# Kernel optimization log

Measured on AMD Instinct MI355X. Metric: run time of the kernel, lower is better.

Reference implementation:

```python
import math
import jax, jax.numpy as jnp
import numpy as np

B = 1024
D = 384
Q = 65536
TOPK = 128
HARD_W = 2.0
TEMP_START = 0.2
TEMP_END = 0.05
WARMUP = 10


def _temperature(epoch):
    # curriculum cosine decay (epoch is a Python int)
    if epoch >= WARMUP:
        return TEMP_END
    progress = epoch / max(1, WARMUP)
    return TEMP_END + 0.5 * (TEMP_START - TEMP_END) * (1.0 + math.cos(math.pi * progress))


def _normalize(x):
    # F.normalize: x / max(||x||, eps)
    n = jnp.linalg.norm(x, axis=-1, keepdims=True)
    return x / jnp.maximum(n, 1e-12)


def _hard_neg_reweight(logits):
    # logits: [B, N]; labels = arange(B) (diagonal positives)
    b = logits.shape[0]
    rows = jnp.arange(b)
    neg_logits = logits.at[rows, rows].set(-jnp.inf)      # mask positives
    _, hard_idx = jax.lax.top_k(neg_logits, TOPK)          # [B, TOPK] hardest negatives
    weights = jnp.ones_like(logits)
    weights = weights.at[rows[:, None], hard_idx].set(HARD_W)
    weights = weights.at[rows, rows].set(1.0)
    return logits * weights


def _cross_entropy_diag(logits):
    b = logits.shape[0]
    logp = jax.nn.log_softmax(logits, axis=-1)
    return -jnp.mean(logp[jnp.arange(b), jnp.arange(b)])


def setup_inputs() -> dict:
    key = jax.random.key(0)
    k1, k2, k3, k4 = jax.random.split(key, 4)
    rgb_feat = jax.random.normal(k1, (B, D), dtype=jnp.float32)
    ir_feat = jax.random.normal(k2, (B, D), dtype=jnp.float32)
    rgb_queue = _normalize(jax.random.normal(k3, (Q, D), dtype=jnp.float32))
    ir_queue = _normalize(jax.random.normal(k4, (Q, D), dtype=jnp.float32))
    return {"rgb_feat": rgb_feat, "ir_feat": ir_feat,
            "rgb_queue": rgb_queue, "ir_queue": ir_queue, "epoch": 0}


def reference(rgb_feat, ir_feat, rgb_queue, ir_queue, epoch):
    temp = _temperature(epoch)
    rgb_z = _normalize(rgb_feat.astype(jnp.float32))
    ir_z = _normalize(ir_feat.astype(jnp.float32))
    ir_all = jnp.concatenate([ir_z, ir_queue], axis=0)    # [B+Q, D]
    rgb_all = jnp.concatenate([rgb_z, rgb_queue], axis=0)
    logits_r2i = (rgb_z @ ir_all.T) / temp                # [B, B+Q]
    logits_i2r = (ir_z @ rgb_all.T) / temp
    logits_r2i = _hard_neg_reweight(logits_r2i)
    logits_i2r = _hard_neg_reweight(logits_i2r)
    return 0.5 * (_cross_entropy_diag(logits_r2i) + _cross_entropy_diag(logits_i2r))
```

## Files before the change

kernel.cpp:

```cpp
#include <hip/hip_runtime.h>
#include <hip/hip_bf16.h>

#define B_    1024
#define D_    384
#define Q_    65536
#define N_    66560
#define TOPK_ 128

#define NBIN_ 4096
#define CAP_  2048

typedef __bf16 bf16x8 __attribute__((ext_vector_type(8)));
typedef float  f32x4  __attribute__((ext_vector_type(4)));
typedef unsigned short u16;
typedef u16 u16x8 __attribute__((ext_vector_type(8)));

__device__ __forceinline__ unsigned short f2bf(float x) {
  unsigned int u = __float_as_uint(x);
  unsigned int r = (u + 0x7fffu + ((u >> 16) & 1u)) >> 16;
  return (unsigned short)r;
}

__device__ __forceinline__ void gld_lds16(const void* g, void* l) {
  __builtin_amdgcn_global_load_lds(
      (__attribute__((address_space(1))) void*)(g),
      (__attribute__((address_space(3))) void*)(l), 16, 0, 0);
}

__device__ __forceinline__ unsigned int bf2key(unsigned int u) {
  return u ^ ((u & 0x8000u) ? 0xFFFFu : 0x8000u);
}

__global__ __launch_bounds__(64) void k_normalize(
    const float* __restrict__ rgb, const float* __restrict__ ir,
    const int* __restrict__ ep,
    u16* __restrict__ zrA, u16* __restrict__ ziA,
    u16* __restrict__ zrU, u16* __restrict__ ziU)
{
  int r = blockIdx.x & (B_ - 1);
  bool isIr = blockIdx.x >= B_;
  const float* src = (isIr ? ir : rgb) + (size_t)r * D_;
  u16* dA = (isIr ? ziA : zrA) + (size_t)r * D_;
  u16* dU = (isIr ? ziU : zrU) + (size_t)r * D_;
  int t = threadIdx.x;
  float x[6]; float ss = 0.f;
  #pragma unroll
  for (int k = 0; k < 6; ++k) { x[k] = src[t + 64*k]; ss += x[k]*x[k]; }
  #pragma unroll
  for (int off = 32; off > 0; off >>= 1) ss += __shfl_down(ss, off);
  ss = __shfl(ss, 0);
  float inv = 1.0f / fmaxf(sqrtf(ss), 1e-12f);

  int e = ep[0];
  float temp;
  if (e >= 10) temp = 0.05f;
  else {
    float p = (float)e * 0.1f;
    temp = 0.05f + 0.075f * (1.0f + cosf(3.14159265358979323846f * p));
  }
  float itemp = 1.0f / temp;

  #pragma unroll
  for (int k = 0; k < 6; ++k) {
    float z = x[k] * inv;
    dU[t + 64*k] = f2bf(z);
    dA[t + 64*k] = f2bf(z * itemp);
  }
}

__global__ __launch_bounds__(256) void k_build_ball(
    const u16* __restrict__ zU, const float* __restrict__ queue,
    u16* __restrict__ ball)
{
  size_t i = ((size_t)blockIdx.x * 256 + threadIdx.x) * 8;
  const size_t zElems = (size_t)B_ * D_;
  if (i < zElems) {
    *(uint4*)(ball + i) = *(const uint4*)(zU + i);
  } else {
    const float* q = queue + (i - zElems);
    float4 a = *(const float4*)q;
    float4 b = *(const float4*)(q + 4);
    u16x8 o;
    o[0] = f2bf(a.x); o[1] = f2bf(a.y); o[2] = f2bf(a.z); o[3] = f2bf(a.w);
    o[4] = f2bf(b.x); o[5] = f2bf(b.y); o[6] = f2bf(b.z); o[7] = f2bf(b.w);
    *(u16x8*)(ball + i) = o;
  }
}

#define BK_ 64
__global__ __launch_bounds__(256) void k_gemm(
    const u16* __restrict__ A,
    const u16* __restrict__ ball,
    u16* __restrict__ C,
    float* __restrict__ diag,
    int r0, int mtiles)
{
  __shared__ u16 As[128 * BK_];
  __shared__ u16 Bs[128 * BK_];

  int bid = blockIdx.x;
  int nwg = gridDim.x;
  int cpx = nwg >> 3;
  int wgid = (bid & 7) * cpx + (bid >> 3);
  int nt = wgid / mtiles;
  int mt = wgid - nt * mtiles;

  const int tid  = threadIdx.x;
  const int wave = tid >> 6, lane = tid & 63;
  const int wm = wave >> 1, wn = wave & 1;
  const int mbase = mt * 128;
  const int nbase = nt * 128;
  const u16* Ab = A    + (size_t)(r0 + mbase) * D_;
  const u16* Bb = ball + (size_t)nbase * D_;

  f32x4 acc[4][4];
  #pragma unroll
  for (int m = 0; m < 4; ++m)
    #pragma unroll
    for (int n = 0; n < 4; ++n)
      #pragma unroll
      for (int r = 0; r < 4; ++r) acc[m][n][r] = 0.0f;

  for (int ks = 0; ks < D_; ks += BK_) {
    #pragma unroll
    for (int i = 0; i < 4; ++i) {
      int f = i * 256 + tid;
      int rr = f >> 3, c = f & 7;
      const u16* ga = Ab + (size_t)rr * D_ + ks + c * 8;
      const u16* gb = Bb + (size_t)rr * D_ + ks + c * 8;
      u16* la = As + (size_t)(i * 256 + wave * 64) * 8;
      u16* lb = Bs + (size_t)(i * 256 + wave * 64) * 8;
      gld_lds16(ga, la);
      gld_lds16(gb, lb);
    }
    __syncthreads();

    const int lr = lane & 15, lk = (lane >> 4) * 8;
    #pragma unroll
    for (int kk = 0; kk < BK_; kk += 32) {
      bf16x8 af[4], bq[4];
      #pragma unroll
      for (int m = 0; m < 4; ++m)
        af[m] = *(const bf16x8*)(As + (wm*64 + m*16 + lr) * BK_ + kk + lk);
      #pragma unroll
      for (int n = 0; n < 4; ++n)
        bq[n] = *(const bf16x8*)(Bs + (wn*64 + n*16 + lr) * BK_ + kk + lk);
      #pragma unroll
      for (int m = 0; m < 4; ++m)
        #pragma unroll
        for (int n = 0; n < 4; ++n)
          acc[m][n] = __builtin_amdgcn_mfma_f32_16x16x32_bf16(af[m], bq[n], acc[m][n], 0, 0, 0);
    }
    __syncthreads();
  }

  const int lr = lane & 15;
  const int rowq = (lane >> 4) * 4;
  #pragma unroll
  for (int m = 0; m < 4; ++m) {
    #pragma unroll
    for (int n = 0; n < 4; ++n) {
      int col = nbase + wn*64 + n*16 + lr;
      #pragma unroll
      for (int r = 0; r < 4; ++r) {
        int srow = mbase + wm*64 + m*16 + rowq + r;
        float x = acc[m][n][r];
        int grow = r0 + srow;
        if (col == grow) { diag[grow] = x; x = -60.0f; }
        C[(size_t)srow * N_ + col] = f2bf(x);
      }
    }
  }
}

__global__ __launch_bounds__(256) void k_select(
    const u16* __restrict__ C, const float* __restrict__ diag,
    float* __restrict__ rowloss, int r0)
{
  __shared__ unsigned int hist[NBIN_];
  __shared__ float vals[CAP_];
  __shared__ float fred[256];
  __shared__ unsigned int csum[256];
  __shared__ int sh_bstar, sh_above, sh_cnt;

  const int t = threadIdx.x;
  const int grow = r0 + blockIdx.x;
  const u16x8* p = (const u16x8*)(C + (size_t)blockIdx.x * N_);

  uint4* h4 = (uint4*)hist;
  #pragma unroll
  for (int i = 0; i < 4; ++i) h4[i * 256 + t] = make_uint4(0,0,0,0);
  if (t == 0) sh_cnt = 0;
  __syncthreads();

  float es0 = 0.f, es1 = 0.f;
  #pragma unroll 1
  for (int base = 0; base < 8192; base += 2048) {
    u16x8 v[8];
    #pragma unroll
    for (int j = 0; j < 8; ++j) v[j] = p[base + j * 256 + t];
    #pragma unroll
    for (int j = 0; j < 8; ++j) {
      #pragma unroll
      for (int e = 0; e < 8; ++e) {
        unsigned int u = (unsigned int)(unsigned short)v[j][e];
        atomicAdd(&hist[bf2key(u) >> 4], 1u);
        float ex = __expf(__uint_as_float(u << 16));
        if (j & 1) es1 += ex; else es0 += ex;
      }
    }
  }
  if (t < 128) {
    u16x8 v = p[8192 + t];
    #pragma unroll
    for (int e = 0; e < 8; ++e) {
      unsigned int u = (unsigned int)(unsigned short)v[e];
      atomicAdd(&hist[bf2key(u) >> 4], 1u);
      es0 += __expf(__uint_as_float(u << 16));
    }
  }
  float esum = es0 + es1;
  __syncthreads();

  unsigned int S = 0;
  #pragma unroll
  for (int i = 0; i < 16; ++i) S += hist[t * 16 + i];
  csum[t] = S;
  __syncthreads();

  unsigned int a = S;
  #pragma unroll
  for (int s = 1; s < 256; s <<= 1) {
    unsigned int add = (t + s < 256) ? csum[t + s] : 0u;
    __syncthreads();
    a += add; csum[t] = a;
    __syncthreads();
  }

  int above_chunk = (t < 255) ? (int)csum[t + 1] : 0;
  if (above_chunk < TOPK_ && above_chunk + (int)S >= TOPK_) {
    int cum = above_chunk;
    #pragma unroll 1
    for (int i = 15; i >= 0; --i) {
      int c = (int)hist[t * 16 + i];
      if (cum + c >= TOPK_) { sh_bstar = t * 16 + i; sh_above = cum; break; }
      cum += c;
    }
  }
  __syncthreads();
  const unsigned int bstar = (unsigned int)sh_bstar;
  const int A = sh_above;

  float delta = 0.f;
  #pragma unroll 1
  for (int base = 0; base < 8192; base += 2048) {
    u16x8 v[8];
    #pragma unroll
    for (int j = 0; j < 8; ++j) v[j] = p[base + j * 256 + t];
    #pragma unroll
    for (int j = 0; j < 8; ++j) {
      #pragma unroll
      for (int e = 0; e < 8; ++e) {
        unsigned int u = (unsigned int)(unsigned short)v[j][e];
        unsigned int bin = bf2key(u) >> 4;
        if (bin >= bstar) {
          float val = __uint_as_float(u << 16);
          if (bin > bstar) delta += __expf(2.f * val) - __expf(val);
          else { int s = atomicAdd(&sh_cnt, 1); if (s < CAP_) vals[s] = val; }
        }
      }
    }
  }
  if (t < 128) {
    u16x8 v = p[8192 + t];
    #pragma unroll
    for (int e = 0; e < 8; ++e) {
      unsigned int u = (unsigned int)(unsigned short)v[e];
      unsigned int bin = bf2key(u) >> 4;
      if (bin >= bstar) {
        float val = __uint_as_float(u << 16);
        if (bin > bstar) delta += __expf(2.f * val) - __expf(val);
        else { int s = atomicAdd(&sh_cnt, 1); if (s < CAP_) vals[s] = val; }
      }
    }
  }
  __syncthreads();

  int C2 = sh_cnt < CAP_ ? sh_cnt : CAP_;
  int need = TOPK_ - A;
  for (int i = t; i < C2; i += 256) {
    float v = vals[i];
    int g = 0;
    for (int k = 0; k < C2; ++k)
      g += (vals[k] > v) || (vals[k] == v && k < i);
    if (g < need) delta += __expf(2.f * v) - __expf(v);
  }

  fred[t] = esum + delta;
  __syncthreads();
  #pragma unroll
  for (int s = 128; s > 0; s >>= 1) { if (t < s) fred[t] += fred[t + s]; __syncthreads(); }

  if (t == 0) {
    float d = diag[grow];
    rowloss[grow] = logf(fred[0] + __expf(d)) - d;
  }
}

__global__ __launch_bounds__(256) void k_final(
    const float* __restrict__ rowloss, float* __restrict__ out)
{
  __shared__ float red[256];
  int t = threadIdx.x;
  float s = 0.f;
  for (int i = t; i < 2 * B_; i += 256) s += rowloss[i];
  red[t] = s;
  __syncthreads();
  for (int k = 128; k > 0; k >>= 1) { if (t < k) red[t] += red[t + k]; __syncthreads(); }
  if (t == 0) out[0] = red[0] * (1.0f / (2.0f * B_));
}

extern "C" void kernel_launch(void* const* d_in, const int* in_sizes, int n_in,
                              void* d_out, int out_size, void* d_ws, size_t ws_size,
                              hipStream_t stream)
{
  const float* rgb_feat = (const float*)d_in[0];
  const float* ir_feat  = (const float*)d_in[1];
  const float* rgb_q    = (const float*)d_in[2];
  const float* ir_q     = (const float*)d_in[3];
  const int*   epoch    = (const int*)d_in[4];

  char* ws = (char*)d_ws;
  size_t off = 0;
  auto alloc = [&](size_t bytes) -> char* {
    char* p = ws + off;
    off = (off + bytes + 255) & ~(size_t)255;
    return p;
  };

  u16* zrA = (u16*)alloc((size_t)B_ * D_ * 2);
  u16* ziA = (u16*)alloc((size_t)B_ * D_ * 2);
  u16* zrU = (u16*)alloc((size_t)B_ * D_ * 2);
  u16* ziU = (u16*)alloc((size_t)B_ * D_ * 2);
  float* diag    = (float*)alloc((size_t)2 * B_ * 4);
  float* rowloss = (float*)alloc((size_t)2 * B_ * 4);
  u16* ball = (u16*)alloc((size_t)N_ * D_ * 2);

  size_t avail = ws_size > off ? ws_size - off : 0;
  int SR = (int)(avail / ((size_t)N_ * 2));
  SR &= ~127;
  if (SR > B_) SR = B_;
  if (SR < 128) SR = 128;
  u16* slab = (u16*)(ws + off);

  k_normalize<<<dim3(2 * B_), dim3(64), 0, stream>>>(
      rgb_feat, ir_feat, epoch, zrA, ziA, zrU, ziU);

  for (int dir = 0; dir < 2; ++dir) {
    const u16*   Amat   = (dir == 0) ? zrA : ziA;
    const u16*   zOther = (dir == 0) ? ziU : zrU;
    const float* queue  = (dir == 0) ? ir_q : rgb_q;
    float* diagD = diag    + dir * B_;
    float* lossD = rowloss + dir * B_;

    k_build_ball<<<dim3((unsigned)((size_t)N_ * D_ / 8 / 256)), dim3(256), 0, stream>>>(
        zOther, queue, ball);

    for (int r0 = 0; r0 < B_; r0 += SR) {
      int cur = (B_ - r0) < SR ? (B_ - r0) : SR;
      int mtiles = cur / 128;
      int nwg = (N_ / 128) * mtiles;
      k_gemm<<<dim3(nwg), dim3(256), 0, stream>>>(
          Amat, ball, slab, diagD, r0, mtiles);
      k_select<<<dim3(cur), dim3(256), 0, stream>>>(slab, diagD, lossD, r0);
    }
  }

  k_final<<<dim3(1), dim3(256), 0, stream>>>(rowloss, (float*)d_out);
}
```

Measured before the change: 367.7 us.

## Load GEMM fragments directly from global and stage output via LDS

```diff
diff --git a/kernel.cpp b/kernel.cpp
--- a/kernel.cpp
+++ b/kernel.cpp
@@ -19,12 +19,6 @@
   unsigned int u = __float_as_uint(x);
   unsigned int r = (u + 0x7fffu + ((u >> 16) & 1u)) >> 16;
   return (unsigned short)r;
-}
-
-__device__ __forceinline__ void gld_lds16(const void* g, void* l) {
-  __builtin_amdgcn_global_load_lds(
-      (__attribute__((address_space(1))) void*)(g),
-      (__attribute__((address_space(3))) void*)(l), 16, 0, 0);
 }
 
 __device__ __forceinline__ unsigned int bf2key(unsigned int u) {
@@ -87,16 +81,14 @@
   }
 }
 
-#define BK_ 64
-__global__ __launch_bounds__(256) void k_gemm(
+__global__ __launch_bounds__(256, 3) void k_gemm(
     const u16* __restrict__ A,
     const u16* __restrict__ ball,
     u16* __restrict__ C,
     float* __restrict__ diag,
     int r0, int mtiles)
 {
-  __shared__ u16 As[128 * BK_];
-  __shared__ u16 Bs[128 * BK_];
+  __shared__ u16 Ct[128 * 136];
 
   int bid = blockIdx.x;
   int nwg = gridDim.x;
@@ -110,8 +102,16 @@
   const int wm = wave >> 1, wn = wave & 1;
   const int mbase = mt * 128;
   const int nbase = nt * 128;
-  const u16* Ab = A    + (size_t)(r0 + mbase) * D_;
-  const u16* Bb = ball + (size_t)nbase * D_;
+  const int lr = lane & 15, lk = (lane >> 4) * 8;
+
+  const u16* pa[4];
+  const u16* pb[4];
+  #pragma unroll
+  for (int m = 0; m < 4; ++m)
+    pa[m] = A + (size_t)(r0 + mbase + wm*64 + m*16 + lr) * D_ + lk;
+  #pragma unroll
+  for (int n = 0; n < 4; ++n)
+    pb[n] = ball + (size_t)(nbase + wn*64 + n*16 + lr) * D_ + lk;
 
   f32x4 acc[4][4];
   #pragma unroll
@@ -121,55 +121,46 @@
       #pragma unroll
       for (int r = 0; r < 4; ++r) acc[m][n][r] = 0.0f;
 
-  for (int ks = 0; ks < D_; ks += BK_) {
-    #pragma unroll
-    for (int i = 0; i < 4; ++i) {
-      int f = i * 256 + tid;
-      int rr = f >> 3, c = f & 7;
-      const u16* ga = Ab + (size_t)rr * D_ + ks + c * 8;
-      const u16* gb = Bb + (size_t)rr * D_ + ks + c * 8;
-      u16* la = As + (size_t)(i * 256 + wave * 64) * 8;
-      u16* lb = Bs + (size_t)(i * 256 + wave * 64) * 8;
-      gld_lds16(ga, la);
-      gld_lds16(gb, lb);
-    }
-    __syncthreads();
-
-    const int lr = lane & 15, lk = (lane >> 4) * 8;
-    #pragma unroll
-    for (int kk = 0; kk < BK_; kk += 32) {
-      bf16x8 af[4], bq[4];
-      #pragma unroll
-      for (int m = 0; m < 4; ++m)
-        af[m] = *(const bf16x8*)(As + (wm*64 + m*16 + lr) * BK_ + kk + lk);
+  #pragma unroll 4
+  for (int kk = 0; kk < D_; kk += 32) {
+    bf16x8 af[4], bq[4];
+    #pragma unroll
+    for (int m = 0; m < 4; ++m) af[m] = *(const bf16x8*)(pa[m] + kk);
+    #pragma unroll
+    for (int n = 0; n < 4; ++n) bq[n] = *(const bf16x8*)(pb[n] + kk);
+    #pragma unroll
+    for (int m = 0; m < 4; ++m)
       #pragma unroll
       for (int n = 0; n < 4; ++n)
-        bq[n] = *(const bf16x8*)(Bs + (wn*64 + n*16 + lr) * BK_ + kk + lk);
-      #pragma unroll
-      for (int m = 0; m < 4; ++m)
-        #pragma unroll
-        for (int n = 0; n < 4; ++n)
-          acc[m][n] = __builtin_amdgcn_mfma_f32_16x16x32_bf16(af[m], bq[n], acc[m][n], 0, 0, 0);
-    }
-    __syncthreads();
-  }
-
-  const int lr = lane & 15;
+        acc[m][n] = __builtin_amdgcn_mfma_f32_16x16x32_bf16(af[m], bq[n], acc[m][n], 0, 0, 0);
+  }
+
   const int rowq = (lane >> 4) * 4;
   #pragma unroll
   for (int m = 0; m < 4; ++m) {
     #pragma unroll
     for (int n = 0; n < 4; ++n) {
-      int col = nbase + wn*64 + n*16 + lr;
+      int lcol = wn*64 + n*16 + lr;
+      int gcol = nbase + lcol;
       #pragma unroll
       for (int r = 0; r < 4; ++r) {
-        int srow = mbase + wm*64 + m*16 + rowq + r;
+        int lrow = wm*64 + m*16 + rowq + r;
         float x = acc[m][n][r];
-        int grow = r0 + srow;
-        if (col == grow) { diag[grow] = x; x = -60.0f; }
-        C[(size_t)srow * N_ + col] = f2bf(x);
+        int grow = r0 + mbase + lrow;
+        if (gcol == grow) { diag[grow] = x; x = -60.0f; }
+        Ct[lrow * 136 + lcol] = f2bf(x);
       }
     }
+  }
+  __syncthreads();
+
+  int rrow = tid >> 4;
+  int cchunk = (tid & 15) * 8;
+  #pragma unroll
+  for (int pass = 0; pass < 8; ++pass) {
+    int row = pass * 16 + rrow;
+    u16x8 v = *(const u16x8*)(Ct + row * 136 + cchunk);
+    *(u16x8*)(C + (size_t)(mbase + row) * N_ + nbase + cchunk) = v;
   }
 }
 
```

Result: slower. 579.2 us (+57.5%).
